# Optimization experiments

Hardware: AMD Instinct MI355X
Metric: run time of the kernel (lower is better)

The kernel has to match this reference:

```python
import jax, jax.numpy as jnp
import numpy as np
import math

HIDDEN = 128; NHEADS = 4; N_COE = 50; N_SCALES = 4; THRE = 5.0; S = 4096; B = 1


def setup_inputs():
    key = jax.random.key(0)
    ks = jax.random.split(key, 12)
    w = lambda k, shape: jax.random.normal(k, shape, jnp.float32) * 0.05
    return {
        "eigenvalue": jax.random.uniform(ks[0], (B, S), jnp.float32) * 2.0,  # graph Laplacian eigvals in [0,2)
        "length": jnp.full((B,), S, dtype=jnp.int32),
        "sele_num": jnp.full((B,), S, dtype=jnp.int32),
        "eig_w_W": w(ks[1], (HIDDEN + 1, HIDDEN)), "eig_w_b": jnp.zeros((HIDDEN,), jnp.float32),
        "mha_ln_g": jnp.ones((HIDDEN,), jnp.float32), "mha_ln_b": jnp.zeros((HIDDEN,), jnp.float32),
        "in_W": w(ks[2], (HIDDEN, 3 * HIDDEN)), "in_b": jnp.zeros((3 * HIDDEN,), jnp.float32),
        "out_W": w(ks[3], (HIDDEN, HIDDEN)), "out_b": jnp.zeros((HIDDEN,), jnp.float32),
        "ffn_ln_g": jnp.ones((HIDDEN,), jnp.float32), "ffn_ln_b": jnp.zeros((HIDDEN,), jnp.float32),
        "ffn1_W": w(ks[4], (HIDDEN, HIDDEN)), "ffn1_b": jnp.zeros((HIDDEN,), jnp.float32),
        "ffn2_W": w(ks[5], (HIDDEN, HIDDEN)), "ffn2_b": jnp.zeros((HIDDEN,), jnp.float32),
        "dsc_W": w(ks[6], (HIDDEN, N_COE)), "dsc_b": jnp.zeros((N_COE,), jnp.float32),
        "dwv_W": w(ks[7], (HIDDEN, N_COE)), "dwv_b": jnp.zeros((N_COE,), jnp.float32),
        "dss_W": w(ks[8], (HIDDEN, N_SCALES)), "dss_b": jnp.zeros((N_SCALES,), jnp.float32),
    }


def layer_norm(x, g, b, eps=1e-5):
    m = x.mean(-1, keepdims=True)
    v = ((x - m) ** 2).mean(-1, keepdims=True)
    return (x - m) / jnp.sqrt(v + eps) * g + b


def sine_encoding(e, W, b):
    # e: [B, S] -> [B, S, HIDDEN]
    div = jnp.exp(jnp.arange(0, HIDDEN, 2, dtype=e.dtype) * (-math.log(10000.0) / HIDDEN))
    pe = (e * 100.0)[..., None] * div  # [B, S, HIDDEN/2]
    eeig = jnp.concatenate([e[..., None], jnp.sin(pe), jnp.cos(pe)], axis=-1)  # [B, S, HIDDEN+1]
    return eeig @ W + b


def mha(x, pad_mask, in_W, in_b, out_W, out_b):
    # x: [B, S, D]; pad_mask: [B, S] True = masked key
    Bb, Ss, D = x.shape
    hd = D // NHEADS
    qkv = x @ in_W + in_b
    q, k, v = jnp.split(qkv, 3, axis=-1)
    hsplit = lambda t: t.reshape(Bb, Ss, NHEADS, hd).transpose(0, 2, 1, 3)  # [B, H, S, hd]
    q, k, v = hsplit(q), hsplit(k), hsplit(v)
    scores = jnp.einsum('bhqd,bhkd->bhqk', q, k) / math.sqrt(hd)
    scores = jnp.where(pad_mask[:, None, None, :], -jnp.inf, scores)
    attn = jax.nn.softmax(scores, axis=-1)
    o = jnp.einsum('bhqk,bhkd->bhqd', attn, v).transpose(0, 2, 1, 3).reshape(Bb, Ss, D)
    return o @ out_W + out_b


def cheb_base(y, n_coe, flag):
    # Chebyshev recurrence: wavelet = [T_0, T_2, ...], scaling = [T_1, T_3, ...]
    te0 = jnp.ones_like(y)
    to0 = y
    def step(carry, _):
        te, to = carry
        te = 2.0 * y * to - te
        to = 2.0 * y * te - to
        return (te, to), (te, to)
    _, (evens, odds) = jax.lax.scan(step, (te0, to0), None, length=n_coe - 1)
    if flag == 'scaling':
        base = jnp.concatenate([to0[None], odds], axis=0)   # [n_coe, B, S, d]
    else:
        base = jnp.concatenate([te0[None], evens], axis=0)
    return jnp.moveaxis(base, 0, 1)  # [B, n_coe, S, d]


def _forward(eigenvalue, eig_w_W, eig_w_b, mha_ln_g, mha_ln_b, in_W, in_b, out_W, out_b,
             ffn_ln_g, ffn_ln_b, ffn1_W, ffn1_b, ffn2_W, ffn2_b,
             dsc_W, dsc_b, dwv_W, dwv_b, dss_W, dss_b, length, sele_num):
    Bb, Ss = eigenvalue.shape
    eve = eigenvalue
    eig_mask = jnp.arange(Ss)[None, :] >= sele_num[:, None]  # [B, S] True = pad
    # --- EigenEncoding (dropout in eval mode = identity) ---
    eig = sine_encoding(eve, eig_w_W, eig_w_b)
    eig = eig + mha(layer_norm(eig, mha_ln_g, mha_ln_b), eig_mask, in_W, in_b, out_W, out_b)
    f = layer_norm(eig, ffn_ln_g, ffn_ln_b)
    f = jax.nn.gelu(f @ ffn1_W + ffn1_b, approximate=False) @ ffn2_W + ffn2_b
    eig_filter = eig + f  # [B, S, HIDDEN]
    lenf = length.astype(eve.dtype)[:, None]
    def pooled(W, b):
        c = eig_filter @ W + b
        c = jnp.where(eig_mask[..., None], 0.0, c)
        return c.sum(axis=1) / (lenf + 1e-8)
    coe_scaling = jax.nn.sigmoid(pooled(dsc_W, dsc_b))
    coe_scaling = coe_scaling / (coe_scaling.sum(-1, keepdims=True) + 1e-8)  # [B, n_coe]
    coe_wavelet = jax.nn.sigmoid(pooled(dwv_W, dwv_b))
    coe_wavelet = coe_wavelet / (coe_wavelet.sum(-1, keepdims=True) + 1e-8)
    coe_scales = jax.nn.sigmoid(pooled(dss_W, dss_b)) * THRE  # [B, n_scales]
    # --- Chebyshev bases ---
    base_scaling = cheb_base(eve[..., None] - 1.0, N_COE, 'scaling')  # [B, n_coe, S, 1]
    fsw = eve[..., None] * coe_scales[:, None, :]                      # [B, S, n_scales]
    fsw = jnp.where(fsw > 2.0, 0.0, fsw)
    base_wavelet = cheb_base(fsw - 1.0, N_COE, 'wavelet')             # [B, n_coe, S, n_scales]
    base_scaling = 0.5 * (1.0 - base_scaling)
    base_wavelet = 0.5 * (1.0 - base_wavelet)
    curr_scaling = jnp.einsum('bc,bcsd->bsd', coe_scaling, base_scaling)
    curr_wavelet = jnp.einsum('bc,bcsd->bsd', coe_wavelet, base_wavelet)
    out = jnp.concatenate([curr_scaling, curr_wavelet], axis=-1)       # [B, S, 1+n_scales]
    out = out / (jnp.linalg.norm(out, axis=-1, keepdims=True) + 1e-8)  # cfg.lam.tight_use = True
    return out


def reference(eigenvalue, length, sele_num, eig_w_W, eig_w_b, mha_ln_g, mha_ln_b, in_W, in_b,
              out_W, out_b, ffn_ln_g, ffn_ln_b, ffn1_W, ffn1_b, ffn2_W, ffn2_b,
              dsc_W, dsc_b, dwv_W, dwv_b, dss_W, dss_b):
    return _forward(eigenvalue, eig_w_W, eig_w_b, mha_ln_g, mha_ln_b, in_W, in_b, out_W, out_b,
                    ffn_ln_g, ffn_ln_b, ffn1_W, ffn1_b, ffn2_W, ffn2_b,
                    dsc_W, dsc_b, dwv_W, dwv_b, dss_W, dss_b, length, sele_num)
```

## Files before the change

kernel.cpp:

```cpp
#include <hip/hip_runtime.h>
#include <hip/hip_bf16.h>
#include <math.h>


#define KSPLIT 4

typedef __attribute__((ext_vector_type(8))) short short8;
typedef __attribute__((ext_vector_type(4))) float f32x4;

__device__ inline unsigned short f2bf(float x) {
    unsigned u = __float_as_uint(x);
    return (unsigned short)((u + 0x7FFFu + ((u >> 16) & 1u)) >> 16);
}
__device__ inline float bf2f(unsigned short h) { return __uint_as_float(((unsigned)h) << 16); }
__device__ inline unsigned pk_bf16(float lo, float hi) {
    __hip_bfloat162 h = __float22bfloat162_rn(make_float2(lo, hi));
    return *reinterpret_cast<unsigned*>(&h);
}

__global__ __launch_bounds__(512) void k_embed(const float* __restrict__ eve,
    const float* __restrict__ eigW, const float* __restrict__ ebias,
    const float* __restrict__ g, const float* __restrict__ b,
    const float* __restrict__ inW, const float* __restrict__ inb,
    float* __restrict__ eig, float* __restrict__ qkv, unsigned short* __restrict__ Khi_g,
    unsigned short* __restrict__ Klo_g, unsigned short* __restrict__ Vt_g,
    float* __restrict__ xsum)
{
    __shared__ __align__(16) float wsh[2][65 * 128];
    __shared__ __align__(16) float se[16][132];
    __shared__ __align__(16) float xn[16][132];
    __shared__ __align__(16) unsigned short vsh[16][136];
    const int t = threadIdx.x;
    const int r0 = blockIdx.x * 16;
    if (blockIdx.x == 0 && t < 128) xsum[t] = 0.f;

    const float4* __restrict__ eigW4 = (const float4*)eigW;
    const float4* __restrict__ inW4  = (const float4*)inW;
    float4 pf0 = eigW4[t];
    float4 pf1 = eigW4[t + 512];
    float4 pf2 = eigW4[t + 1024];
    float4 pf3 = eigW4[t + 1536];
    float4 pf4;
    if (t < 32) pf4 = eigW4[t + 2048];

    {
        const int rr = t >> 5, l5 = t & 31;
        const float e = eve[r0 + rr];
        if (l5 == 0) se[rr][128] = e;
        #pragma unroll
        for (int jj = 0; jj < 2; ++jj) {
            const int j = l5 * 2 + jj;
            const float div = __expf(-0.07195578415606394f * (float)(2 * j));
            const float pe = e * 100.0f * div;
            se[rr][j]      = __sinf(pe);
            se[rr][64 + j] = __cosf(pe);
        }
    }
    {
        float4* dst = (float4*)wsh[0];
        dst[t] = pf0; dst[t + 512] = pf1; dst[t + 1024] = pf2; dst[t + 1536] = pf3;
        if (t < 32) dst[t + 2048] = pf4;
    }
    const int r  = t >> 5;
    const int c0 = (t & 31) * 4;
    const int kb = t >> 5, c4 = t & 31;
    float a0, a1, a2, a3;
    float xa[4];

    __syncthreads();
    pf0 = eigW4[2080 + t];        pf1 = eigW4[2080 + t + 512];
    pf2 = eigW4[2080 + t + 1024]; pf3 = eigW4[2080 + t + 1536];
    {
        const float* __restrict__ W = wsh[0];
        const float4 w0 = *(const float4*)&W[c0];
        const float ea = se[r][128];
        a0 = ea * w0.x; a1 = ea * w0.y; a2 = ea * w0.z; a3 = ea * w0.w;
        #pragma unroll 8
        for (int k = 0; k < 64; ++k) {
            const float xv = se[r][k];
            const float4 wk = *(const float4*)&W[(k + 1) * 128 + c0];
            a0 = fmaf(xv, wk.x, a0); a1 = fmaf(xv, wk.y, a1);
            a2 = fmaf(xv, wk.z, a2); a3 = fmaf(xv, wk.w, a3);
        }
    }
    {   float4* dst = (float4*)wsh[1];
        dst[t] = pf0; dst[t + 512] = pf1; dst[t + 1024] = pf2; dst[t + 1536] = pf3;
    }
    __syncthreads();
    pf0 = inW4[(size_t)(kb +  0) * 96 + c4];
    pf1 = inW4[(size_t)(kb + 16) * 96 + c4];
    pf2 = inW4[(size_t)(kb + 32) * 96 + c4];
    pf3 = inW4[(size_t)(kb + 48) * 96 + c4];
    {
        const float* __restrict__ W = wsh[1];
        #pragma unroll 8
        for (int k = 64; k < 128; ++k) {
            const float xv = se[r][k];
            const float4 wk = *(const float4*)&W[(k - 64) * 128 + c0];
            a0 = fmaf(xv, wk.x, a0); a1 = fmaf(xv, wk.y, a1);
            a2 = fmaf(xv, wk.z, a2); a3 = fmaf(xv, wk.w, a3);
        }
        const float4 bb = *(const float4*)&ebias[c0];
        xa[0] = a0 + bb.x; xa[1] = a1 + bb.y; xa[2] = a2 + bb.z; xa[3] = a3 + bb.w;
        *(float4*)&eig[(size_t)(r0 + r) * 128 + c0] = make_float4(xa[0], xa[1], xa[2], xa[3]);
        float sa = (xa[0] + xa[1]) + (xa[2] + xa[3]);
        float qa = (xa[0] * xa[0] + xa[1] * xa[1]) + (xa[2] * xa[2] + xa[3] * xa[3]);
        #pragma unroll
        for (int m = 1; m < 32; m <<= 1) {
            sa += __shfl_xor(sa, m, 32); qa += __shfl_xor(qa, m, 32);
        }
        const float ma = sa * (1.f / 128.f);
        const float ia = 1.f / sqrtf(qa * (1.f / 128.f) - ma * ma + 1e-5f);
        const float4 gg = *(const float4*)&g[c0];
        const float4 lb = *(const float4*)&b[c0];
        *(float4*)&xn[r][c0] = make_float4((xa[0] - ma) * ia * gg.x + lb.x,
                                           (xa[1] - ma) * ia * gg.y + lb.y,
                                           (xa[2] - ma) * ia * gg.z + lb.z,
                                           (xa[3] - ma) * ia * gg.w + lb.w);
    }
    {   float4* dst = (float4*)wsh[0];
        dst[t] = pf0; dst[t + 512] = pf1; dst[t + 1024] = pf2; dst[t + 1536] = pf3;
    }
    const int row = r0 + r;
    float A0, A1, A2, A3;
    #pragma unroll
    for (int p = 0; p < 3; ++p) {
        #pragma unroll
        for (int hh = 0; hh < 2; ++hh) {
            __syncthreads();
            const bool last = (p == 2 && hh == 1);
            if (!last) {
                const int np = p + hh, nh = hh ^ 1;
                pf0 = inW4[(size_t)(kb +  0 + nh * 64) * 96 + np * 32 + c4];
                pf1 = inW4[(size_t)(kb + 16 + nh * 64) * 96 + np * 32 + c4];
                pf2 = inW4[(size_t)(kb + 32 + nh * 64) * 96 + np * 32 + c4];
                pf3 = inW4[(size_t)(kb + 48 + nh * 64) * 96 + np * 32 + c4];
            }
            if (hh == 0) {
                const float4 bb = *(const float4*)&inb[p * 128 + c0];
                A0 = bb.x; A1 = bb.y; A2 = bb.z; A3 = bb.w;
            }
            const float* __restrict__ W = wsh[hh];
            #pragma unroll 8
            for (int k2 = 0; k2 < 64; ++k2) {
                const float xv = xn[r][hh * 64 + k2];
                const float4 wk = *(const float4*)&W[k2 * 128 + c0];
                A0 = fmaf(xv, wk.x, A0); A1 = fmaf(xv, wk.y, A1);
                A2 = fmaf(xv, wk.z, A2); A3 = fmaf(xv, wk.w, A3);
            }
            if (!last) {
                float4* dst = (float4*)wsh[hh ^ 1];
                dst[t] = pf0; dst[t + 512] = pf1; dst[t + 1024] = pf2; dst[t + 1536] = pf3;
            }
            if (hh == 1) {
                if (p == 0) {
                    *(float4*)&qkv[(size_t)row * 384 + c0] = make_float4(A0, A1, A2, A3);
                } else if (p == 1) {
                    const int h = c0 >> 5, d = c0 & 31;
                    float A[4] = {A0, A1, A2, A3};
                    unsigned short h4[4], l4v[4];
                    #pragma unroll
                    for (int i = 0; i < 4; ++i) { h4[i] = f2bf(A[i]); l4v[i] = f2bf(A[i] - bf2f(h4[i])); }
                    *(uint2*)&Khi_g[((size_t)h * 4096 + row) * 32 + d] = *(uint2*)h4;
                    *(uint2*)&Klo_g[((size_t)h * 4096 + row) * 32 + d] = *(uint2*)l4v;
                } else {
                    unsigned short v4[4];
                    float A[4] = {A0, A1, A2, A3};
                    #pragma unroll
                    for (int i = 0; i < 4; ++i) v4[i] = f2bf(A[i]);
                    *(uint2*)&vsh[r][c0] = *(uint2*)v4;
                }
            }
        }
    }
    __syncthreads();
    if (t < 128) {
        __align__(16) unsigned short tmp[16];
        #pragma unroll
        for (int k2 = 0; k2 < 16; ++k2) tmp[k2] = vsh[k2][t];
        *(uint4*)&Vt_g[(size_t)t * 4096 + r0]     = *(uint4*)&tmp[0];
        *(uint4*)&Vt_g[(size_t)t * 4096 + r0 + 8] = *(uint4*)&tmp[8];
    }
}

#define KSTR 40
#define VSTR 72
#define PSTR 72

__global__ __launch_bounds__(256) void k_attn(const float* __restrict__ qkv,
    const unsigned short* __restrict__ Khi_g, const unsigned short* __restrict__ Klo_g,
    const unsigned short* __restrict__ Vt_g,
    const int* __restrict__ sele, float* __restrict__ Oe, float* __restrict__ E)
{
    __shared__ __align__(16) unsigned short Khi[2][64 * KSTR];
    __shared__ __align__(16) unsigned short Klo[2][64 * KSTR];
    __shared__ __align__(16) unsigned short Vt[2][32 * VSTR];
    __shared__ __align__(16) unsigned short Pb[4][16 * PSTR];

    const int t = threadIdx.x;
    const int lane = t & 63;
    const int l = lane & 15;
    const int quad = lane >> 4;
    const int wv = __builtin_amdgcn_readfirstlane(t >> 6);
    const int qb = blockIdx.x;
    const int h  = blockIdx.y;
    const int ks = blockIdx.z;
    const int nk = sele[0];

    short8 qhi, qlo;
    {
        const float* __restrict__ qr = qkv + (size_t)(qb * 64 + wv * 16 + l) * 384 + h * 32 + quad * 8;
        const float4 a = *(const float4*)qr;
        const float4 b = *(const float4*)(qr + 4);
        const float sc = 0.17677669529663687f;
        float v[8] = {a.x * sc, a.y * sc, a.z * sc, a.w * sc, b.x * sc, b.y * sc, b.z * sc, b.w * sc};
        #pragma unroll
        for (int j = 0; j < 8; ++j) {
            const unsigned short hb = f2bf(v[j]);
            qhi[j] = (short)hb;
            qlo[j] = (short)f2bf(v[j] - bf2f(hb));
        }
    }
    f32x4 accO0 = {0.f, 0.f, 0.f, 0.f};
    f32x4 accO1 = {0.f, 0.f, 0.f, 0.f};
    float elane = 0.f;

    const int kk = t >> 2;
    const int d0 = (t & 3) * 8;
    const int vd = t >> 3;
    const int ko = (t & 7) * 8;

    const unsigned short* __restrict__ pKhi = Khi_g + ((size_t)h * 4096 + ks * 1024 + kk) * 32 + d0;
    const unsigned short* __restrict__ pKlo = Klo_g + ((size_t)h * 4096 + ks * 1024 + kk) * 32 + d0;
    const unsigned short* __restrict__ pVt  = Vt_g  + ((size_t)h * 32 + vd) * 4096 + ks * 1024 + ko;

    uint4 kh_n = *(const uint4*)pKhi;
    uint4 kl_n = *(const uint4*)pKlo;
    uint4 vv_n = *(const uint4*)pVt;
    *(uint4*)&Khi[0][kk * KSTR + d0] = kh_n;
    *(uint4*)&Klo[0][kk * KSTR + d0] = kl_n;
    *(uint4*)&Vt[0][vd * VSTR + ko]  = vv_n;

    for (int ch = 0; ch < 16; ++ch) {
        __syncthreads();
        const int cur = ch & 1;
        if (ch < 15) {
            kh_n = *(const uint4*)(pKhi + (size_t)(ch + 1) * 2048);
            kl_n = *(const uint4*)(pKlo + (size_t)(ch + 1) * 2048);
            vv_n = *(const uint4*)(pVt  + (ch + 1) * 64);
        }
        const int keybase = ks * 1024 + ch * 64;
        const unsigned short* __restrict__ KhiC = Khi[cur];
        const unsigned short* __restrict__ KloC = Klo[cur];
        const unsigned short* __restrict__ VtC  = Vt[cur];
        unsigned short* __restrict__ Pw = Pb[wv];
        #pragma unroll
        for (int tile = 0; tile < 4; ++tile) {
            const int kl = tile * 16 + l;
            const short8 kh = *(const short8*)&KhiC[kl * KSTR + quad * 8];
            const short8 kw = *(const short8*)&KloC[kl * KSTR + quad * 8];
            f32x4 S = {0.f, 0.f, 0.f, 0.f};
            __builtin_amdgcn_s_setprio(1);
            S = __builtin_amdgcn_mfma_f32_16x16x32_bf16(kh, qhi, S, 0, 0, 0);
            S = __builtin_amdgcn_mfma_f32_16x16x32_bf16(kw, qhi, S, 0, 0, 0);
            S = __builtin_amdgcn_mfma_f32_16x16x32_bf16(kh, qlo, S, 0, 0, 0);
            __builtin_amdgcn_s_setprio(0);
            const int kg0 = keybase + tile * 16 + quad * 4;
            const float p0 = (kg0 + 0 < nk) ? __expf(S[0]) : 0.f;
            const float p1 = (kg0 + 1 < nk) ? __expf(S[1]) : 0.f;
            const float p2 = (kg0 + 2 < nk) ? __expf(S[2]) : 0.f;
            const float p3 = (kg0 + 3 < nk) ? __expf(S[3]) : 0.f;
            elane += (p0 + p1) + (p2 + p3);
            *(uint2*)&Pw[l * PSTR + tile * 16 + quad * 4] =
                make_uint2(pk_bf16(p0, p1), pk_bf16(p2, p3));
        }
        #pragma unroll
        for (int step = 0; step < 2; ++step) {
            const short8 pa  = *(const short8*)&Pw[l * PSTR + step * 32 + quad * 8];
            const short8 vb0 = *(const short8*)&VtC[l * VSTR + step * 32 + quad * 8];
            const short8 vb1 = *(const short8*)&VtC[(16 + l) * VSTR + step * 32 + quad * 8];
            __builtin_amdgcn_s_setprio(1);
            accO0 = __builtin_amdgcn_mfma_f32_16x16x32_bf16(pa, vb0, accO0, 0, 0, 0);
            accO1 = __builtin_amdgcn_mfma_f32_16x16x32_bf16(pa, vb1, accO1, 0, 0, 0);
            __builtin_amdgcn_s_setprio(0);
        }
        if (ch < 15) {
            *(uint4*)&Khi[cur ^ 1][kk * KSTR + d0] = kh_n;
            *(uint4*)&Klo[cur ^ 1][kk * KSTR + d0] = kl_n;
            *(uint4*)&Vt[cur ^ 1][vd * VSTR + ko]  = vv_n;
        }
    }
    elane += __shfl_xor(elane, 16, 64);
    elane += __shfl_xor(elane, 32, 64);
    const int qrow0 = qb * 64 + wv * 16;
    if (lane < 16)
        E[((size_t)ks * 4 + h) * 4096 + qrow0 + l] = elane;
    #pragma unroll
    for (int r = 0; r < 4; ++r) {
        const size_t row = qrow0 + quad * 4 + r;
        Oe[((size_t)ks * 4096 + row) * 128 + h * 32 + l]      = accO0[r];
        Oe[((size_t)ks * 4096 + row) * 128 + h * 32 + 16 + l] = accO1[r];
    }
}

__global__ __launch_bounds__(512) void k_ffn(const float* __restrict__ eig,
    const float* __restrict__ Oe, const float* __restrict__ E,
    const float* __restrict__ outW, const float* __restrict__ outb,
    const float* __restrict__ lg, const float* __restrict__ lb,
    const float* __restrict__ W1, const float* __restrict__ b1,
    const float* __restrict__ W2, const float* __restrict__ b2,
    const int* __restrict__ sele, float* __restrict__ xsum)
{
    __shared__ __align__(16) float wsh[2][64 * 128];
    __shared__ __align__(16) float sA[16][132];
    __shared__ __align__(16) float xn[16][132];
    __shared__ __align__(16) float cs[16][132];
    const int t = threadIdx.x;
    const int r0 = blockIdx.x * 16;
    const int r  = t >> 5;
    const int c0 = (t & 31) * 4;

    const float4* __restrict__ Wp0 = (const float4*)outW;
    const float4* __restrict__ Wp1 = (const float4*)W1;
    const float4* __restrict__ Wp2 = (const float4*)W2;

    float4 pf0 = Wp0[t], pf1 = Wp0[t + 512], pf2 = Wp0[t + 1024], pf3 = Wp0[t + 1536];

    {
        const int h = c0 >> 5;
        float es = 0.f;
        float v[4] = {0.f, 0.f, 0.f, 0.f};
        #pragma unroll
        for (int ks = 0; ks < KSPLIT; ++ks) {
            es += E[((size_t)ks * 4 + h) * 4096 + r0 + r];
            const float4 o1 = *(const float4*)&Oe[((size_t)ks * 4096 + r0 + r) * 128 + c0];
            v[0] += o1.x; v[1] += o1.y; v[2] += o1.z; v[3] += o1.w;
        }
        const float rcp = 1.f / es;
        *(float4*)&sA[r][c0] = make_float4(v[0] * rcp, v[1] * rcp, v[2] * rcp, v[3] * rcp);
    }
    {   float4* dst = (float4*)wsh[0];
        dst[t] = pf0; dst[t + 512] = pf1; dst[t + 1024] = pf2; dst[t + 1536] = pf3;
    }

    float x2[4];
    float A0, A1, A2, A3;
    #pragma unroll
    for (int gphase = 0; gphase < 6; ++gphase) {
        const int gg = gphase >> 1, hh = gphase & 1;
        __syncthreads();
        if (gphase < 5) {
            const int nid = gphase + 1;
            const int ng = nid >> 1, nh = nid & 1;
            const float4* __restrict__ src = (ng == 0) ? Wp0 : (ng == 1 ? Wp1 : Wp2);
            pf0 = src[nh * 2048 + t];        pf1 = src[nh * 2048 + t + 512];
            pf2 = src[nh * 2048 + t + 1024]; pf3 = src[nh * 2048 + t + 1536];
        }
        if (hh == 0) {
            const float* bias = (gg == 0) ? outb : (gg == 1 ? b1 : b2);
            const float4 bb = *(const float4*)&bias[c0];
            A0 = bb.x; A1 = bb.y; A2 = bb.z; A3 = bb.w;
        }
        const float* __restrict__ W = wsh[hh];
        const float* __restrict__ act = (gg == 1) ? &xn[r][0] : &sA[r][0];
        #pragma unroll 8
        for (int k2 = 0; k2 < 64; ++k2) {
            const float xv = act[hh * 64 + k2];
            const float4 wk = *(const float4*)&W[k2 * 128 + c0];
            A0 = fmaf(xv, wk.x, A0); A1 = fmaf(xv, wk.y, A1);
            A2 = fmaf(xv, wk.z, A2); A3 = fmaf(xv, wk.w, A3);
        }
        if (gphase < 5) {
            float4* dst = (float4*)wsh[hh ^ 1];
            dst[t] = pf0; dst[t + 512] = pf1; dst[t + 1024] = pf2; dst[t + 1536] = pf3;
        }
        if (hh == 1) {
            if (gg == 0) {
                const float4 ea = *(const float4*)&eig[(size_t)(r0 + r) * 128 + c0];
                x2[0] = ea.x + A0; x2[1] = ea.y + A1; x2[2] = ea.z + A2; x2[3] = ea.w + A3;
                float sa = (x2[0] + x2[1]) + (x2[2] + x2[3]);
                float qa = (x2[0] * x2[0] + x2[1] * x2[1]) + (x2[2] * x2[2] + x2[3] * x2[3]);
                #pragma unroll
                for (int m = 1; m < 32; m <<= 1) {
                    sa += __shfl_xor(sa, m, 32); qa += __shfl_xor(qa, m, 32);
                }
                const float ma = sa * (1.f / 128.f);
                const float ia = 1.f / sqrtf(qa * (1.f / 128.f) - ma * ma + 1e-5f);
                const float4 gg4 = *(const float4*)&lg[c0];
                const float4 bb4 = *(const float4*)&lb[c0];
                *(float4*)&xn[r][c0] = make_float4((x2[0] - ma) * ia * gg4.x + bb4.x,
                                                   (x2[1] - ma) * ia * gg4.y + bb4.y,
                                                   (x2[2] - ma) * ia * gg4.z + bb4.z,
                                                   (x2[3] - ma) * ia * gg4.w + bb4.w);
            } else if (gg == 1) {
                *(float4*)&sA[r][c0] = make_float4(
                    0.5f * A0 * (1.f + erff(A0 * 0.70710678118654752f)),
                    0.5f * A1 * (1.f + erff(A1 * 0.70710678118654752f)),
                    0.5f * A2 * (1.f + erff(A2 * 0.70710678118654752f)),
                    0.5f * A3 * (1.f + erff(A3 * 0.70710678118654752f)));
            } else {
                const int nsel = sele[0];
                const bool ina = (r0 + r) < nsel;
                *(float4*)&cs[r][c0] = ina ? make_float4(x2[0] + A0, x2[1] + A1, x2[2] + A2, x2[3] + A3)
                                           : make_float4(0.f, 0.f, 0.f, 0.f);
            }
        }
    }
    __syncthreads();
    if (t < 128) {
        float s = 0.f;
        #pragma unroll
        for (int rr = 0; rr < 16; ++rr) s += cs[rr][t];
        atomicAdd(&xsum[t], s);
    }
}

__global__ __launch_bounds__(128) void k_tail(const float* __restrict__ eve,
    const float* __restrict__ xsum,
    const float* __restrict__ dscW, const float* __restrict__ dscb,
    const float* __restrict__ dwvW, const float* __restrict__ dwvb,
    const float* __restrict__ dssW, const float* __restrict__ dssb,
    const int* __restrict__ len, const int* __restrict__ sele,
    float* __restrict__ out)
{
    __shared__ float xs[128];
    __shared__ float val[104];
    __shared__ float s2[2];
    __shared__ float csc[50], cwv[50], cssh[4];
    __shared__ float sv[16][6];
    const int t = threadIdx.x;
    xs[t] = xsum[t];
    __syncthreads();
    if (t < 104) {
        const float invl = 1.f / ((float)len[0] + 1e-8f);
        const float ns = (float)sele[0];
        const float* Wp; int stride, col; float bias;
        if (t < 50)       { Wp = dscW; stride = 50; col = t;       bias = dscb[t]; }
        else if (t < 100) { Wp = dwvW; stride = 50; col = t - 50;  bias = dwvb[t - 50]; }
        else              { Wp = dssW; stride = 4;  col = t - 100; bias = dssb[t - 100]; }
        float a = 0.f;
        #pragma unroll 4
        for (int k = 0; k < 128; ++k) a = fmaf(xs[k], Wp[k * stride + col], a);
        a = (a + ns * bias) * invl;
        val[t] = 1.f / (1.f + __expf(-a));
    }
    __syncthreads();
    if (t == 0) { float s = 0.f; for (int i = 0; i < 50; ++i) s += val[i]; s2[0] = s; }
    if (t == 1) { float s = 0.f; for (int i = 0; i < 50; ++i) s += val[50 + i]; s2[1] = s; }
    __syncthreads();
    if (t < 50) {
        csc[t] = val[t] / (s2[0] + 1e-8f);
        cwv[t] = val[50 + t] / (s2[1] + 1e-8f);
    } else if (t >= 100 && t < 104) {
        cssh[t - 100] = val[t] * 5.0f;
    }
    __syncthreads();
    const int e_i = t / 5, c = t - e_i * 5;
    if (t < 80) {
        const float e = eve[blockIdx.x * 16 + e_i];
        float y;
        if (c == 0) y = e - 1.f;
        else { float f = e * cssh[c - 1]; if (f > 2.f) f = 0.f; y = f - 1.f; }
        const float* __restrict__ cf = (c == 0) ? csc : cwv;
        float te = 1.f, to = y;
        float u = (c == 0) ? to : te;
        float a = cf[0] * (0.5f * (1.f - u));
        const float y2 = 2.f * y;
        for (int i = 1; i < 50; ++i) {
            te = fmaf(y2, to, -te);
            to = fmaf(y2, te, -to);
            u = (c == 0) ? to : te;
            a = fmaf(cf[i], 0.5f * (1.f - u), a);
        }
        sv[e_i][c] = a;
    }
    __syncthreads();
    if (t < 80) {
        float n2 = 0.f;
        #pragma unroll
        for (int k = 0; k < 5; ++k) n2 += sv[e_i][k] * sv[e_i][k];
        const float invn = 1.f / (sqrtf(n2) + 1e-8f);
        out[(size_t)(blockIdx.x * 16 + e_i) * 5 + c] = sv[e_i][c] * invn;
    }
}

extern "C" void kernel_launch(void* const* d_in, const int* in_sizes, int n_in,
                              void* d_out, int out_size, void* d_ws, size_t ws_size,
                              hipStream_t stream) {
    const float* eve  = (const float*)d_in[0];
    const int*   len  = (const int*)d_in[1];
    const int*   sele = (const int*)d_in[2];
    const float* eigW = (const float*)d_in[3];
    const float* eigB = (const float*)d_in[4];
    const float* mlg  = (const float*)d_in[5];
    const float* mlb  = (const float*)d_in[6];
    const float* inW  = (const float*)d_in[7];
    const float* inb  = (const float*)d_in[8];
    const float* outW = (const float*)d_in[9];
    const float* outb = (const float*)d_in[10];
    const float* flg  = (const float*)d_in[11];
    const float* flb  = (const float*)d_in[12];
    const float* W1   = (const float*)d_in[13];
    const float* b1   = (const float*)d_in[14];
    const float* W2   = (const float*)d_in[15];
    const float* b2   = (const float*)d_in[16];
    const float* dscW = (const float*)d_in[17];
    const float* dscb = (const float*)d_in[18];
    const float* dwvW = (const float*)d_in[19];
    const float* dwvb = (const float*)d_in[20];
    const float* dssW = (const float*)d_in[21];
    const float* dssb = (const float*)d_in[22];

    float* ws   = (float*)d_ws;
    float* eig  = ws;
    float* qkv  = ws + 524288;
    float* Oe   = ws + 2097152;
    float* E    = ws + 4194304;
    float* xsum = ws + 4259840;
    unsigned short* Khi_g = (unsigned short*)(ws + 4260352);
    unsigned short* Klo_g = (unsigned short*)(ws + 4522496);
    unsigned short* Vt_g  = (unsigned short*)(ws + 4784640);
    float* out  = (float*)d_out;

    k_embed<<<256, 512, 0, stream>>>(eve, eigW, eigB, mlg, mlb, inW, inb,
                                     eig, qkv, Khi_g, Klo_g, Vt_g, xsum);
    k_attn <<<dim3(64, 4, KSPLIT), 256, 0, stream>>>(qkv, Khi_g, Klo_g, Vt_g, sele, Oe, E);
    k_ffn  <<<256, 512, 0, stream>>>(eig, Oe, E, outW, outb, flg, flb, W1, b1, W2, b2, sele, xsum);
    k_tail <<<256, 128, 0, stream>>>(eve, xsum, dscW, dscb, dwvW, dwvb, dssW, dssb, len, sele, out);
}
```

Baseline: 179.5 us.

## Load K/V attention operands straight into registers, drop LDS staging and barriers

The attention kernel no longer stages K-hi/K-lo/V tiles through double-buffered shared memory with a __syncthreads per chunk. Each wave now loads its MFMA operand fragments directly from global memory into registers, prefetching the next chunk's K fragments. A separate unmasked fast path skips the per-key bounds check when the whole chunk is valid. This removes LDS traffic and block barriers, but each of the four waves now reads the same K/V from global or L2 on its own, and register pressure rises.

New measurement: 210.5 us. 1.17x slower.

```diff
diff --git a/kernel.cpp b/kernel.cpp
--- a/kernel.cpp
+++ b/kernel.cpp
@@ -183,18 +183,32 @@
     }
 }
 
-#define KSTR 40
-#define VSTR 72
 #define PSTR 72
+
+#define QK_TILES_REG(MASKED)                                                      \
+    _Pragma("unroll")                                                             \
+    for (int tile = 0; tile < 4; ++tile) {                                        \
+        f32x4 S = {0.f, 0.f, 0.f, 0.f};                                           \
+        __builtin_amdgcn_s_setprio(1);                                            \
+        S = __builtin_amdgcn_mfma_f32_16x16x32_bf16(khc[tile], qhi, S, 0, 0, 0);  \
+        S = __builtin_amdgcn_mfma_f32_16x16x32_bf16(kwc[tile], qhi, S, 0, 0, 0);  \
+        S = __builtin_amdgcn_mfma_f32_16x16x32_bf16(khc[tile], qlo, S, 0, 0, 0);  \
+        __builtin_amdgcn_s_setprio(0);                                            \
+        const int kg0 = keybase + tile * 16 + quad * 4;                           \
+        const float p0 = (!(MASKED) || (kg0 + 0 < nk)) ? __expf(S[0]) : 0.f;      \
+        const float p1 = (!(MASKED) || (kg0 + 1 < nk)) ? __expf(S[1]) : 0.f;      \
+        const float p2 = (!(MASKED) || (kg0 + 2 < nk)) ? __expf(S[2]) : 0.f;      \
+        const float p3 = (!(MASKED) || (kg0 + 3 < nk)) ? __expf(S[3]) : 0.f;      \
+        elane += (p0 + p1) + (p2 + p3);                                           \
+        *(uint2*)&Pw[l * PSTR + tile * 16 + quad * 4] =                           \
+            make_uint2(pk_bf16(p0, p1), pk_bf16(p2, p3));                         \
+    }
 
 __global__ __launch_bounds__(256) void k_attn(const float* __restrict__ qkv,
     const unsigned short* __restrict__ Khi_g, const unsigned short* __restrict__ Klo_g,
     const unsigned short* __restrict__ Vt_g,
     const int* __restrict__ sele, float* __restrict__ Oe, float* __restrict__ E)
 {
-    __shared__ __align__(16) unsigned short Khi[2][64 * KSTR];
-    __shared__ __align__(16) unsigned short Klo[2][64 * KSTR];
-    __shared__ __align__(16) unsigned short Vt[2][32 * VSTR];
     __shared__ __align__(16) unsigned short Pb[4][16 * PSTR];
 
     const int t = threadIdx.x;
@@ -225,69 +239,54 @@
     f32x4 accO1 = {0.f, 0.f, 0.f, 0.f};
     float elane = 0.f;
 
-    const int kk = t >> 2;
-    const int d0 = (t & 3) * 8;
-    const int vd = t >> 3;
-    const int ko = (t & 7) * 8;
-
-    const unsigned short* __restrict__ pKhi = Khi_g + ((size_t)h * 4096 + ks * 1024 + kk) * 32 + d0;
-    const unsigned short* __restrict__ pKlo = Klo_g + ((size_t)h * 4096 + ks * 1024 + kk) * 32 + d0;
-    const unsigned short* __restrict__ pVt  = Vt_g  + ((size_t)h * 32 + vd) * 4096 + ks * 1024 + ko;
-
-    uint4 kh_n = *(const uint4*)pKhi;
-    uint4 kl_n = *(const uint4*)pKlo;
-    uint4 vv_n = *(const uint4*)pVt;
-    *(uint4*)&Khi[0][kk * KSTR + d0] = kh_n;
-    *(uint4*)&Klo[0][kk * KSTR + d0] = kl_n;
-    *(uint4*)&Vt[0][vd * VSTR + ko]  = vv_n;
+    const size_t kofs0 = ((size_t)h * 4096 + ks * 1024 + l) * 32 + quad * 8;
+    const unsigned short* __restrict__ pKhi = Khi_g + kofs0;
+    const unsigned short* __restrict__ pKlo = Klo_g + kofs0;
+    const size_t vofs0 = ((size_t)h * 32 + l) * 4096 + ks * 1024 + quad * 8;
+    const unsigned short* __restrict__ pV0 = Vt_g + vofs0;
+    const unsigned short* __restrict__ pV1 = Vt_g + vofs0 + (size_t)16 * 4096;
+
+    unsigned short* __restrict__ Pw = Pb[wv];
+
+    short8 khc[4], kwc[4], khn[4], kwn[4];
+    #pragma unroll
+    for (int tile = 0; tile < 4; ++tile) {
+        khc[tile] = *(const short8*)(pKhi + (size_t)(tile * 16) * 32);
+        kwc[tile] = *(const short8*)(pKlo + (size_t)(tile * 16) * 32);
+    }
 
     for (int ch = 0; ch < 16; ++ch) {
-        __syncthreads();
-        const int cur = ch & 1;
+        const int keybase = ks * 1024 + ch * 64;
         if (ch < 15) {
-            kh_n = *(const uint4*)(pKhi + (size_t)(ch + 1) * 2048);
-            kl_n = *(const uint4*)(pKlo + (size_t)(ch + 1) * 2048);
-            vv_n = *(const uint4*)(pVt  + (ch + 1) * 64);
-        }
-        const int keybase = ks * 1024 + ch * 64;
-        const unsigned short* __restrict__ KhiC = Khi[cur];
-        const unsigned short* __restrict__ KloC = Klo[cur];
-        const unsigned short* __restrict__ VtC  = Vt[cur];
-        unsigned short* __restrict__ Pw = Pb[wv];
+            #pragma unroll
+            for (int tile = 0; tile < 4; ++tile) {
+                khn[tile] = *(const short8*)(pKhi + (size_t)((ch + 1) * 64 + tile * 16) * 32);
+                kwn[tile] = *(const short8*)(pKlo + (size_t)((ch + 1) * 64 + tile * 16) * 32);
+            }
+        }
+        short8 vb0[2], vb1[2];
+        #pragma unroll
+        for (int step = 0; step < 2; ++step) {
+            vb0[step] = *(const short8*)(pV0 + ch * 64 + step * 32);
+            vb1[step] = *(const short8*)(pV1 + ch * 64 + step * 32);
+        }
+        if (keybase + 64 <= nk) {
+            QK_TILES_REG(0)
+        } else {
+            QK_TILES_REG(1)
+        }
+        #pragma unroll
+        for (int step = 0; step < 2; ++step) {
+            const short8 pa = *(const short8*)&Pw[l * PSTR + step * 32 + quad * 8];
+            __builtin_amdgcn_s_setprio(1);
+            accO0 = __builtin_amdgcn_mfma_f32_16x16x32_bf16(pa, vb0[step], accO0, 0, 0, 0);
+            accO1 = __builtin_amdgcn_mfma_f32_16x16x32_bf16(pa, vb1[step], accO1, 0, 0, 0);
+            __builtin_amdgcn_s_setprio(0);
+        }
         #pragma unroll
         for (int tile = 0; tile < 4; ++tile) {
-            const int kl = tile * 16 + l;
-            const short8 kh = *(const short8*)&KhiC[kl * KSTR + quad * 8];
-            const short8 kw = *(const short8*)&KloC[kl * KSTR + quad * 8];
-            f32x4 S = {0.f, 0.f, 0.f, 0.f};
-            __builtin_amdgcn_s_setprio(1);
-            S = __builtin_amdgcn_mfma_f32_16x16x32_bf16(kh, qhi, S, 0, 0, 0);
-            S = __builtin_amdgcn_mfma_f32_16x16x32_bf16(kw, qhi, S, 0, 0, 0);
-            S = __builtin_amdgcn_mfma_f32_16x16x32_bf16(kh, qlo, S, 0, 0, 0);
-            __builtin_amdgcn_s_setprio(0);
-            const int kg0 = keybase + tile * 16 + quad * 4;
-            const float p0 = (kg0 + 0 < nk) ? __expf(S[0]) : 0.f;
-            const float p1 = (kg0 + 1 < nk) ? __expf(S[1]) : 0.f;
-            const float p2 = (kg0 + 2 < nk) ? __expf(S[2]) : 0.f;
-            const float p3 = (kg0 + 3 < nk) ? __expf(S[3]) : 0.f;
-            elane += (p0 + p1) + (p2 + p3);
-            *(uint2*)&Pw[l * PSTR + tile * 16 + quad * 4] =
-                make_uint2(pk_bf16(p0, p1), pk_bf16(p2, p3));
-        }
-        #pragma unroll
-        for (int step = 0; step < 2; ++step) {
-            const short8 pa  = *(const short8*)&Pw[l * PSTR + step * 32 + quad * 8];
-            const short8 vb0 = *(const short8*)&VtC[l * VSTR + step * 32 + quad * 8];
-            const short8 vb1 = *(const short8*)&VtC[(16 + l) * VSTR + step * 32 + quad * 8];
-            __builtin_amdgcn_s_setprio(1);
-            accO0 = __builtin_amdgcn_mfma_f32_16x16x32_bf16(pa, vb0, accO0, 0, 0, 0);
-            accO1 = __builtin_amdgcn_mfma_f32_16x16x32_bf16(pa, vb1, accO1, 0, 0, 0);
-            __builtin_amdgcn_s_setprio(0);
-        }
-        if (ch < 15) {
-            *(uint4*)&Khi[cur ^ 1][kk * KSTR + d0] = kh_n;
-            *(uint4*)&Klo[cur ^ 1][kk * KSTR + d0] = kl_n;
-            *(uint4*)&Vt[cur ^ 1][vd * VSTR + ko]  = vv_n;
+            khc[tile] = khn[tile];
+            kwc[tile] = kwn[tile];
         }
     }
     elane += __shfl_xor(elane, 16, 64);
```
